# Kernel optimization log

Hardware: AMD Instinct MI355X
Metric: run time of the kernel (lower is better)

The kernel has to match this reference:

```python
import jax, jax.numpy as jnp
import numpy as np

B, H, T, D = 4, 16, 1024, 64
M = H * D  # model_dim = 1024
P = 2 * T - 1  # relative position length


def rel_shift(x):
    # x: (B, H, T, 2T-1) -> (B, H, T, T)
    b, h, t1, p = x.shape
    zero_pad = jnp.zeros((b, h, t1, 1), dtype=x.dtype)
    x_padded = jnp.concatenate([zero_pad, x], axis=-1)        # (B,H,T,2T)
    x_padded = x_padded.reshape(b, h, p + 1, t1)              # (B,H,2T,T)
    x = x_padded[:, :, 1:].reshape(b, h, t1, p)               # (B,H,T,2T-1)
    return x[:, :, :, : p // 2 + 1]                           # (B,H,T,T)


def setup_inputs() -> dict:
    key = jax.random.key(0)
    ks = jax.random.split(key, 7)
    q = jax.random.normal(ks[0], (B, H, T, D), dtype=jnp.float32)
    k = jax.random.normal(ks[1], (B, H, T, D), dtype=jnp.float32)
    v = jax.random.normal(ks[2], (B, H, T, D), dtype=jnp.float32)
    pos_emb = jax.random.normal(ks[3], (1, P, M), dtype=jnp.float32)
    attention_mask = jnp.ones((B, 1, 1, T), dtype=bool)
    # learned params
    W_pos = jax.random.normal(ks[4], (M, M), dtype=jnp.float32) * (M ** -0.5)
    pos_bias_u = jax.random.normal(ks[5], (H, D), dtype=jnp.float32) * 0.02
    pos_bias_v = jax.random.normal(ks[6], (H, D), dtype=jnp.float32) * 0.02
    return {"q": q, "k": k, "v": v, "pos_emb": pos_emb,
            "attention_mask": attention_mask, "W_pos": W_pos,
            "pos_bias_u": pos_bias_u, "pos_bias_v": pos_bias_v}


def reference(q, k, v, pos_emb, attention_mask, W_pos, pos_bias_u, pos_bias_v):
    # q, k, v: (B, H, T, D); pos_emb: (1, P, M)
    q_u = q + pos_bias_u[None, :, None, :]
    q_v = q + pos_bias_v[None, :, None, :]
    # linear_pos (no bias), split heads: (1, H, P, D)
    p = (pos_emb @ W_pos.T).reshape(pos_emb.shape[0], -1, H, D).transpose(0, 2, 1, 3)
    matrix_ac = jnp.einsum('bhqd,bhkd->bhqk', q_u, k)          # (B,H,T,T)
    matrix_bd = jnp.einsum('bhqd,hpd->bhqp', q_v, p[0])        # (B,H,T,P)
    matrix_bd = rel_shift(matrix_bd)                           # (B,H,T,T)
    scale = q.shape[-1] ** -0.5
    sim = (matrix_ac + matrix_bd) * scale
    sim = jnp.where(attention_mask, sim, jnp.finfo(sim.dtype).min)
    attn = jax.nn.softmax(sim, axis=-1)
    return jnp.einsum('bhqk,bhkd->bhqd', attn, v)
```

## Files before the change

kernel.cpp:

```cpp
#include <hip/hip_runtime.h>
#include <hip/hip_bf16.h>

#define BB 4
#define HH 16
#define TT 1024
#define DD 64
#define PP 2047
#define MM 1024

typedef __bf16 bf16;
typedef __bf16 bf16x8 __attribute__((ext_vector_type(8)));
typedef float  f32x4  __attribute__((ext_vector_type(4)));

__device__ inline bf16x8 pack8(float4 a, float4 b) {
    bf16x8 r;
    r[0]=(bf16)a.x; r[1]=(bf16)a.y; r[2]=(bf16)a.z; r[3]=(bf16)a.w;
    r[4]=(bf16)b.x; r[5]=(bf16)b.y; r[6]=(bf16)b.z; r[7]=(bf16)b.w;
    return r;
}

__device__ inline bf16x8 pack8_add_scale(float4 a, float4 b, float4 c, float4 d, float s) {
    bf16x8 r;
    r[0]=(bf16)((a.x+c.x)*s); r[1]=(bf16)((a.y+c.y)*s); r[2]=(bf16)((a.z+c.z)*s); r[3]=(bf16)((a.w+c.w)*s);
    r[4]=(bf16)((b.x+d.x)*s); r[5]=(bf16)((b.y+d.y)*s); r[6]=(bf16)((b.z+d.z)*s); r[7]=(bf16)((b.w+d.w)*s);
    return r;
}

__global__ __launch_bounds__(256) void cast_bf16_kernel(const float* __restrict__ src,
                                                        bf16* __restrict__ dst, int n8) {
    int i = blockIdx.x * 256 + threadIdx.x;
    if (i >= n8) return;
    const float4* s = (const float4*)src + (size_t)i * 2;
    ((bf16x8*)dst)[i] = pack8(s[0], s[1]);
}

__global__ __launch_bounds__(256) void transpose_v_kernel(const float* __restrict__ v,
                                                          bf16* __restrict__ vt) {
    __shared__ __attribute__((aligned(16))) bf16 Tld[64][72];
    const int t = threadIdx.x;
    const int bh = blockIdx.y;
    const int t0 = blockIdx.x * 64;
    {
        const int r = t >> 2, c0 = (t & 3) * 16;
        const float4* src = (const float4*)(v + ((size_t)bh * TT + t0 + r) * DD + c0);
        float4 a = src[0], b = src[1], c = src[2], d = src[3];
        *(bf16x8*)&Tld[r][c0]     = pack8(a, b);
        *(bf16x8*)&Tld[r][c0 + 8] = pack8(c, d);
    }
    __syncthreads();
    const int dd = t >> 2, j0l = (t & 3) * 16;
    bf16x8 o0, o1;
#pragma unroll
    for (int i = 0; i < 8; ++i) o0[i] = Tld[j0l + i][dd];
#pragma unroll
    for (int i = 0; i < 8; ++i) o1[i] = Tld[j0l + 8 + i][dd];
    bf16* dst = vt + ((size_t)bh * DD + dd) * TT + t0 + j0l;
    *(bf16x8*)dst = o0;
    *(bf16x8*)(dst + 8) = o1;
}

__global__ __launch_bounds__(256) void pos_gemm_kernel(const float* __restrict__ pos_emb,
                                                       const float* __restrict__ W_pos,
                                                       bf16* __restrict__ p_bf) {
    __shared__ __attribute__((aligned(16))) bf16 Abuf[64][72];
    __shared__ __attribute__((aligned(16))) bf16 Bbuf[128][72];
    const int t = threadIdx.x;
    const int w = t >> 6, lane = t & 63, quad = lane >> 4, col = lane & 15;
    const int wr = w >> 1, wc = w & 1;
    const int pp0 = blockIdx.x * 64;
    const int n0 = blockIdx.y * 128;

    f32x4 acc[2][4];
#pragma unroll
    for (int i = 0; i < 2; ++i)
#pragma unroll
        for (int j = 0; j < 4; ++j) acc[i][j] = (f32x4){0.f,0.f,0.f,0.f};

    for (int kt = 0; kt < 16; ++kt) {
        const int k0 = kt * 64;
        __syncthreads();
        {
            const int row = t >> 2, ch = (t & 3) * 16;
            const int pp = pp0 + row;
            if (pp < PP) {
                const float4* s = (const float4*)(pos_emb + (size_t)pp * MM + k0 + ch);
                float4 a = s[0], b = s[1], c = s[2], d = s[3];
                *(bf16x8*)&Abuf[row][ch]     = pack8(a, b);
                *(bf16x8*)&Abuf[row][ch + 8] = pack8(c, d);
            } else {
                float4 z = make_float4(0.f,0.f,0.f,0.f);
                *(bf16x8*)&Abuf[row][ch]     = pack8(z, z);
                *(bf16x8*)&Abuf[row][ch + 8] = pack8(z, z);
            }
        }
#pragma unroll
        for (int c = 0; c < 2; ++c) {
            const int idx = t * 2 + c;
            const int row = idx >> 2, ch = (idx & 3) * 16;
            const float4* s = (const float4*)(W_pos + (size_t)(n0 + row) * MM + k0 + ch);
            float4 a = s[0], b = s[1], cc = s[2], d = s[3];
            *(bf16x8*)&Bbuf[row][ch]     = pack8(a, b);
            *(bf16x8*)&Bbuf[row][ch + 8] = pack8(cc, d);
        }
        __syncthreads();
#pragma unroll
        for (int mt = 0; mt < 2; ++mt) {
            const int ar = wr * 32 + mt * 16 + col;
            const bf16x8 a0 = *(const bf16x8*)&Abuf[ar][quad * 8];
            const bf16x8 a1 = *(const bf16x8*)&Abuf[ar][32 + quad * 8];
#pragma unroll
            for (int nt = 0; nt < 4; ++nt) {
                const int br = wc * 64 + nt * 16 + col;
                const bf16x8 b0 = *(const bf16x8*)&Bbuf[br][quad * 8];
                const bf16x8 b1 = *(const bf16x8*)&Bbuf[br][32 + quad * 8];
                acc[mt][nt] = __builtin_amdgcn_mfma_f32_16x16x32_bf16(a0, b0, acc[mt][nt], 0, 0, 0);
                acc[mt][nt] = __builtin_amdgcn_mfma_f32_16x16x32_bf16(a1, b1, acc[mt][nt], 0, 0, 0);
            }
        }
    }
#pragma unroll
    for (int mt = 0; mt < 2; ++mt)
#pragma unroll
        for (int nt = 0; nt < 4; ++nt)
#pragma unroll
            for (int reg = 0; reg < 4; ++reg) {
                const int pp = pp0 + wr * 32 + mt * 16 + quad * 4 + reg;
                if (pp < PP) {
                    const int n = n0 + wc * 64 + nt * 16 + col;
                    p_bf[((size_t)(n >> 6) * PP + pp) * DD + (n & 63)] = (bf16)acc[mt][nt][reg];
                }
            }
}

__global__ __launch_bounds__(256, 4) void flash_kernel(const float* __restrict__ q,
                                                       const bf16* __restrict__ k_bf,
                                                       const bf16* __restrict__ vt_g,
                                                       const bf16* __restrict__ p_bf,
                                                       const float* __restrict__ bias_u,
                                                       const float* __restrict__ bias_v,
                                                       float* __restrict__ out) {
    __shared__ __attribute__((aligned(16))) bf16 Kld[64][72];
    __shared__ __attribute__((aligned(16))) bf16 Vt[64][72];
    __shared__ __attribute__((aligned(16))) bf16 Pwin[128][72];

    const int t = threadIdx.x;
    const int w = t >> 6, lane = t & 63, quad = lane >> 4, col = lane & 15;
    const int id = blockIdx.x;
    const int bh = ((id >> 7) << 3) | (id & 7);
    const int i0 = ((id >> 3) & 15) * 64;
    const int h = bh & 15;

    const float c1 = 0.18033688011112042f;

    bf16x8 quf[2], qvf[2];
    {
        const int rg = i0 + 16 * w + col;
        const float* qrow = q + ((size_t)bh * TT + rg) * DD;
        const float* urow = bias_u + h * DD;
        const float* vrow = bias_v + h * DD;
#pragma unroll
        for (int kk = 0; kk < 2; ++kk) {
            int off = kk * 32 + quad * 8;
            float4 f0 = *(const float4*)(qrow + off);
            float4 f1 = *(const float4*)(qrow + off + 4);
            float4 u0 = *(const float4*)(urow + off);
            float4 u1 = *(const float4*)(urow + off + 4);
            float4 v0 = *(const float4*)(vrow + off);
            float4 v1 = *(const float4*)(vrow + off + 4);
            quf[kk] = pack8_add_scale(f0, f1, u0, u1, c1);
            qvf[kk] = pack8_add_scale(f0, f1, v0, v1, c1);
        }
    }

    f32x4 acc[4] = {{0.f,0.f,0.f,0.f},{0.f,0.f,0.f,0.f},{0.f,0.f,0.f,0.f},{0.f,0.f,0.f,0.f}};
    float lpart[4] = {0.f, 0.f, 0.f, 0.f};

    const int sr = t >> 2, sc = (t & 3) * 16;

    for (int j0 = 0; j0 < TT; j0 += 64) {
        const int w0j = (TT - 64) + j0 - i0;
        __syncthreads();
        {
            const bf16x8* src = (const bf16x8*)(k_bf + ((size_t)bh * TT + j0 + sr) * DD + sc);
            *(bf16x8*)&Kld[sr][sc]     = src[0];
            *(bf16x8*)&Kld[sr][sc + 8] = src[1];
        }
#pragma unroll
        for (int c = 0; c < 2; ++c) {
            const int idx = t * 2 + c;
            const int dd = idx >> 3, ch = (idx & 7) * 8;
            *(bf16x8*)&Vt[dd][ch] =
                *(const bf16x8*)(vt_g + ((size_t)bh * DD + dd) * TT + j0 + ch);
        }
        if (j0 == 0) {
#pragma unroll
            for (int c = 0; c < 4; ++c) {
                const int idx = t * 4 + c;
                const int row = idx >> 3, ch = (idx & 7) * 8;
                const int pp = w0j + row;
                const int phys = pp & 127;
                if (pp < PP) {
                    *(bf16x8*)&Pwin[phys][ch] =
                        *(const bf16x8*)(p_bf + ((size_t)h * PP + pp) * DD + ch);
                } else {
                    float4 z = make_float4(0.f,0.f,0.f,0.f);
                    *(bf16x8*)&Pwin[phys][ch] = pack8(z, z);
                }
            }
        } else {
#pragma unroll
            for (int c = 0; c < 2; ++c) {
                const int idx = t * 2 + c;
                const int row = idx >> 3, ch = (idx & 7) * 8;
                const int pp = w0j + 64 + row;
                const int phys = pp & 127;
                if (pp < PP) {
                    *(bf16x8*)&Pwin[phys][ch] =
                        *(const bf16x8*)(p_bf + ((size_t)h * PP + pp) * DD + ch);
                } else {
                    float4 z = make_float4(0.f,0.f,0.f,0.f);
                    *(bf16x8*)&Pwin[phys][ch] = pack8(z, z);
                }
            }
        }
        __syncthreads();

        f32x4 s[4];
#pragma unroll
        for (int jt = 0; jt < 4; ++jt) {
            bf16x8 b0 = *(const bf16x8*)&Kld[jt * 16 + col][quad * 8];
            bf16x8 b1 = *(const bf16x8*)&Kld[jt * 16 + col][32 + quad * 8];
            f32x4 z = {0.f,0.f,0.f,0.f};
            z = __builtin_amdgcn_mfma_f32_16x16x32_bf16(quf[0], b0, z, 0, 0, 0);
            z = __builtin_amdgcn_mfma_f32_16x16x32_bf16(quf[1], b1, z, 0, 0, 0);
            s[jt] = z;
        }

        f32x4 zf[5];
#pragma unroll
        for (int f = 0; f < 5; ++f) {
            const int pp = w0j + (3 - w + f) * 16 + col;
            const int phys = pp & 127;
            bf16x8 b0 = *(const bf16x8*)&Pwin[phys][quad * 8];
            bf16x8 b1 = *(const bf16x8*)&Pwin[phys][32 + quad * 8];
            f32x4 z = {0.f,0.f,0.f,0.f};
            z = __builtin_amdgcn_mfma_f32_16x16x32_bf16(qvf[0], b0, z, 0, 0, 0);
            z = __builtin_amdgcn_mfma_f32_16x16x32_bf16(qvf[1], b1, z, 0, 0, 0);
            zf[f] = z;
        }

#pragma unroll
        for (int reg = 0; reg < 4; ++reg) {
            const int rl = quad * 4 + reg;
            const int srcc = (col + 15 - rl) & 15;
            const int idx = (((lane & 48) | srcc) << 2);
            float pm[5];
#pragma unroll
            for (int f = 0; f < 5; ++f)
                pm[f] = __int_as_float(__builtin_amdgcn_ds_bpermute(idx, __float_as_int(zf[f][reg])));
            const bool low = (col <= rl);
#pragma unroll
            for (int jt = 0; jt < 4; ++jt) {
                float x = s[jt][reg] + (low ? pm[jt] : pm[jt + 1]);
                float pv = exp2f(x);
                s[jt][reg] = pv;
                lpart[reg] += pv;
            }
        }
        __syncthreads();
#pragma unroll
        for (int reg = 0; reg < 4; ++reg) {
            const int rl = quad * 4 + reg;
#pragma unroll
            for (int jt = 0; jt < 4; ++jt)
                Kld[16 * w + rl][jt * 16 + col] = (bf16)s[jt][reg];
        }

#pragma unroll
        for (int kk = 0; kk < 2; ++kk) {
            bf16x8 af = *(const bf16x8*)&Kld[16 * w + col][kk * 32 + quad * 8];
#pragma unroll
            for (int jt = 0; jt < 4; ++jt) {
                bf16x8 bfv = *(const bf16x8*)&Vt[jt * 16 + col][kk * 32 + quad * 8];
                acc[jt] = __builtin_amdgcn_mfma_f32_16x16x32_bf16(af, bfv, acc[jt], 0, 0, 0);
            }
        }
    }

#pragma unroll
    for (int reg = 0; reg < 4; ++reg) {
        float lt = lpart[reg];
#pragma unroll
        for (int off = 1; off < 16; off <<= 1) lt += __shfl_xor(lt, off, 64);
        const float inv = 1.0f / lt;
        const int rg = i0 + 16 * w + quad * 4 + reg;
#pragma unroll
        for (int jt = 0; jt < 4; ++jt)
            out[((size_t)bh * TT + rg) * DD + jt * 16 + col] = acc[jt][reg] * inv;
    }
}

extern "C" void kernel_launch(void* const* d_in, const int* in_sizes, int n_in,
                              void* d_out, int out_size, void* d_ws, size_t ws_size,
                              hipStream_t stream) {
    const float* q       = (const float*)d_in[0];
    const float* k       = (const float*)d_in[1];
    const float* v       = (const float*)d_in[2];
    const float* pos_emb = (const float*)d_in[3];
    const float* W_pos   = (const float*)d_in[5];
    const float* bias_u  = (const float*)d_in[6];
    const float* bias_v  = (const float*)d_in[7];
    float* out = (float*)d_out;

    char* ws = (char*)d_ws;
    bf16* k_bf = (bf16*)(ws);
    bf16* vt_g = (bf16*)(ws + 8388608);
    bf16* p_bf = (bf16*)(ws + 16777216);

    const int n8 = (BB * HH * TT * DD) / 8;
    cast_bf16_kernel<<<n8 / 256, 256, 0, stream>>>(k, k_bf, n8);
    transpose_v_kernel<<<dim3(16, 64), 256, 0, stream>>>(v, vt_g);
    pos_gemm_kernel<<<dim3(32, 8), 256, 0, stream>>>(pos_emb, W_pos, p_bf);
    flash_kernel<<<1024, 256, 0, stream>>>(q, k_bf, vt_g, p_bf, bias_u, bias_v, out);
}
```

Baseline: 206.4 us.

## Give each wave 32 query rows and read K, V, P straight from global

Result: slower. 254.7 us (+23.4%).

```diff
diff --git a/kernel.cpp b/kernel.cpp
--- a/kernel.cpp
+++ b/kernel.cpp
@@ -132,29 +132,31 @@
             }
 }
 
-__global__ __launch_bounds__(256, 4) void flash_kernel(const float* __restrict__ q,
+__global__ __launch_bounds__(256, 3) void flash_kernel(const float* __restrict__ q,
                                                        const bf16* __restrict__ k_bf,
                                                        const bf16* __restrict__ vt_g,
                                                        const bf16* __restrict__ p_bf,
                                                        const float* __restrict__ bias_u,
                                                        const float* __restrict__ bias_v,
                                                        float* __restrict__ out) {
-    __shared__ __attribute__((aligned(16))) bf16 Kld[64][72];
-    __shared__ __attribute__((aligned(16))) bf16 Vt[64][72];
-    __shared__ __attribute__((aligned(16))) bf16 Pwin[128][72];
+    __shared__ __attribute__((aligned(16))) bf16 Sp[4][32][72];
 
     const int t = threadIdx.x;
     const int w = t >> 6, lane = t & 63, quad = lane >> 4, col = lane & 15;
     const int id = blockIdx.x;
-    const int bh = ((id >> 7) << 3) | (id & 7);
-    const int i0 = ((id >> 3) & 15) * 64;
+    const int bh = ((id >> 6) << 3) | (id & 7);
+    const int i0 = ((id >> 3) & 7) * 128;
     const int h = bh & 15;
 
     const float c1 = 0.18033688011112042f;
 
-    bf16x8 quf[2], qvf[2];
-    {
-        const int rg = i0 + 16 * w + col;
+    const int rs0 = i0 + 32 * w;
+    const int rs1 = rs0 + 16;
+
+    bf16x8 qu[2][2], qv[2][2];
+#pragma unroll
+    for (int s_ = 0; s_ < 2; ++s_) {
+        const int rg = rs0 + 16 * s_ + col;
         const float* qrow = q + ((size_t)bh * TT + rg) * DD;
         const float* urow = bias_u + h * DD;
         const float* vrow = bias_v + h * DD;
@@ -167,137 +169,111 @@
             float4 u1 = *(const float4*)(urow + off + 4);
             float4 v0 = *(const float4*)(vrow + off);
             float4 v1 = *(const float4*)(vrow + off + 4);
-            quf[kk] = pack8_add_scale(f0, f1, u0, u1, c1);
-            qvf[kk] = pack8_add_scale(f0, f1, v0, v1, c1);
+            qu[s_][kk] = pack8_add_scale(f0, f1, u0, u1, c1);
+            qv[s_][kk] = pack8_add_scale(f0, f1, v0, v1, c1);
         }
     }
 
-    f32x4 acc[4] = {{0.f,0.f,0.f,0.f},{0.f,0.f,0.f,0.f},{0.f,0.f,0.f,0.f},{0.f,0.f,0.f,0.f}};
-    float lpart[4] = {0.f, 0.f, 0.f, 0.f};
-
-    const int sr = t >> 2, sc = (t & 3) * 16;
+    f32x4 acc[2][4];
+#pragma unroll
+    for (int s_ = 0; s_ < 2; ++s_)
+#pragma unroll
+        for (int jt = 0; jt < 4; ++jt) acc[s_][jt] = (f32x4){0.f,0.f,0.f,0.f};
+    float lpart[2][4] = {{0.f,0.f,0.f,0.f},{0.f,0.f,0.f,0.f}};
+
+    const int srcc = (col + 15) & 15;
 
     for (int j0 = 0; j0 < TT; j0 += 64) {
-        const int w0j = (TT - 64) + j0 - i0;
-        __syncthreads();
-        {
-            const bf16x8* src = (const bf16x8*)(k_bf + ((size_t)bh * TT + j0 + sr) * DD + sc);
-            *(bf16x8*)&Kld[sr][sc]     = src[0];
-            *(bf16x8*)&Kld[sr][sc + 8] = src[1];
-        }
-#pragma unroll
-        for (int c = 0; c < 2; ++c) {
-            const int idx = t * 2 + c;
-            const int dd = idx >> 3, ch = (idx & 7) * 8;
-            *(bf16x8*)&Vt[dd][ch] =
-                *(const bf16x8*)(vt_g + ((size_t)bh * DD + dd) * TT + j0 + ch);
-        }
-        if (j0 == 0) {
-#pragma unroll
-            for (int c = 0; c < 4; ++c) {
-                const int idx = t * 4 + c;
-                const int row = idx >> 3, ch = (idx & 7) * 8;
-                const int pp = w0j + row;
-                const int phys = pp & 127;
-                if (pp < PP) {
-                    *(bf16x8*)&Pwin[phys][ch] =
-                        *(const bf16x8*)(p_bf + ((size_t)h * PP + pp) * DD + ch);
-                } else {
-                    float4 z = make_float4(0.f,0.f,0.f,0.f);
-                    *(bf16x8*)&Pwin[phys][ch] = pack8(z, z);
+        f32x4 s[2][4];
+#pragma unroll
+        for (int jt = 0; jt < 4; ++jt) {
+            const bf16* kr = k_bf + ((size_t)bh * TT + j0 + jt * 16 + col) * DD + quad * 8;
+            bf16x8 kb0 = *(const bf16x8*)kr;
+            bf16x8 kb1 = *(const bf16x8*)(kr + 32);
+            f32x4 z0 = {0.f,0.f,0.f,0.f};
+            z0 = __builtin_amdgcn_mfma_f32_16x16x32_bf16(qu[0][0], kb0, z0, 0, 0, 0);
+            z0 = __builtin_amdgcn_mfma_f32_16x16x32_bf16(qu[0][1], kb1, z0, 0, 0, 0);
+            s[0][jt] = z0;
+            f32x4 z1 = {0.f,0.f,0.f,0.f};
+            z1 = __builtin_amdgcn_mfma_f32_16x16x32_bf16(qu[1][0], kb0, z1, 0, 0, 0);
+            z1 = __builtin_amdgcn_mfma_f32_16x16x32_bf16(qu[1][1], kb1, z1, 0, 0, 0);
+            s[1][jt] = z1;
+        }
+
+        const int fb = (TT - 16) + j0 - rs1;
+        f32x4 zf1[5], zf0[5];
+#pragma unroll
+        for (int f = 0; f < 6; ++f) {
+            int pp = fb + 16 * f + col;
+            pp = min(max(pp, 0), PP - 1);
+            const bf16* pr = p_bf + ((size_t)h * PP + pp) * DD + quad * 8;
+            bf16x8 pb0 = *(const bf16x8*)pr;
+            bf16x8 pb1 = *(const bf16x8*)(pr + 32);
+            if (f < 5) {
+                f32x4 z = {0.f,0.f,0.f,0.f};
+                z = __builtin_amdgcn_mfma_f32_16x16x32_bf16(qv[1][0], pb0, z, 0, 0, 0);
+                z = __builtin_amdgcn_mfma_f32_16x16x32_bf16(qv[1][1], pb1, z, 0, 0, 0);
+                zf1[f] = z;
+            }
+            if (f >= 1) {
+                f32x4 z = {0.f,0.f,0.f,0.f};
+                z = __builtin_amdgcn_mfma_f32_16x16x32_bf16(qv[0][0], pb0, z, 0, 0, 0);
+                z = __builtin_amdgcn_mfma_f32_16x16x32_bf16(qv[0][1], pb1, z, 0, 0, 0);
+                zf0[f - 1] = z;
+            }
+        }
+
+#pragma unroll
+        for (int s_ = 0; s_ < 2; ++s_) {
+#pragma unroll
+            for (int reg = 0; reg < 4; ++reg) {
+                const int rl = quad * 4 + reg;
+                const int sc2 = (col + 15 - rl) & 15;
+                const int idx = (((lane & 48) | sc2) << 2);
+                float pm[5];
+#pragma unroll
+                for (int f = 0; f < 5; ++f) {
+                    const f32x4& zz = s_ ? zf1[f] : zf0[f];
+                    pm[f] = __int_as_float(__builtin_amdgcn_ds_bpermute(idx, __float_as_int(zz[reg])));
                 }
-            }
-        } else {
-#pragma unroll
-            for (int c = 0; c < 2; ++c) {
-                const int idx = t * 2 + c;
-                const int row = idx >> 3, ch = (idx & 7) * 8;
-                const int pp = w0j + 64 + row;
-                const int phys = pp & 127;
-                if (pp < PP) {
-                    *(bf16x8*)&Pwin[phys][ch] =
-                        *(const bf16x8*)(p_bf + ((size_t)h * PP + pp) * DD + ch);
-                } else {
-                    float4 z = make_float4(0.f,0.f,0.f,0.f);
-                    *(bf16x8*)&Pwin[phys][ch] = pack8(z, z);
+                const bool low = (col <= rl);
+#pragma unroll
+                for (int jt = 0; jt < 4; ++jt) {
+                    float x = s[s_][jt][reg] + (low ? pm[jt] : pm[jt + 1]);
+                    float pv = exp2f(x);
+                    lpart[s_][reg] += pv;
+                    Sp[w][16 * s_ + rl][jt * 16 + col] = (bf16)pv;
                 }
             }
         }
-        __syncthreads();
-
-        f32x4 s[4];
-#pragma unroll
-        for (int jt = 0; jt < 4; ++jt) {
-            bf16x8 b0 = *(const bf16x8*)&Kld[jt * 16 + col][quad * 8];
-            bf16x8 b1 = *(const bf16x8*)&Kld[jt * 16 + col][32 + quad * 8];
-            f32x4 z = {0.f,0.f,0.f,0.f};
-            z = __builtin_amdgcn_mfma_f32_16x16x32_bf16(quf[0], b0, z, 0, 0, 0);
-            z = __builtin_amdgcn_mfma_f32_16x16x32_bf16(quf[1], b1, z, 0, 0, 0);
-            s[jt] = z;
-        }
-
-        f32x4 zf[5];
-#pragma unroll
-        for (int f = 0; f < 5; ++f) {
-            const int pp = w0j + (3 - w + f) * 16 + col;
-            const int phys = pp & 127;
-            bf16x8 b0 = *(const bf16x8*)&Pwin[phys][quad * 8];
-            bf16x8 b1 = *(const bf16x8*)&Pwin[phys][32 + quad * 8];
-            f32x4 z = {0.f,0.f,0.f,0.f};
-            z = __builtin_amdgcn_mfma_f32_16x16x32_bf16(qvf[0], b0, z, 0, 0, 0);
-            z = __builtin_amdgcn_mfma_f32_16x16x32_bf16(qvf[1], b1, z, 0, 0, 0);
-            zf[f] = z;
-        }
-
+
+#pragma unroll
+        for (int kk = 0; kk < 2; ++kk) {
+            bf16x8 af0 = *(const bf16x8*)&Sp[w][col][kk * 32 + quad * 8];
+            bf16x8 af1 = *(const bf16x8*)&Sp[w][16 + col][kk * 32 + quad * 8];
+#pragma unroll
+            for (int jt = 0; jt < 4; ++jt) {
+                const bf16* vr = vt_g + ((size_t)bh * DD + jt * 16 + col) * TT + j0 + kk * 32 + quad * 8;
+                bf16x8 vb = *(const bf16x8*)vr;
+                acc[0][jt] = __builtin_amdgcn_mfma_f32_16x16x32_bf16(af0, vb, acc[0][jt], 0, 0, 0);
+                acc[1][jt] = __builtin_amdgcn_mfma_f32_16x16x32_bf16(af1, vb, acc[1][jt], 0, 0, 0);
+            }
+        }
+    }
+
+#pragma unroll
+    for (int s_ = 0; s_ < 2; ++s_)
 #pragma unroll
         for (int reg = 0; reg < 4; ++reg) {
-            const int rl = quad * 4 + reg;
-            const int srcc = (col + 15 - rl) & 15;
-            const int idx = (((lane & 48) | srcc) << 2);
-            float pm[5];
-#pragma unroll
-            for (int f = 0; f < 5; ++f)
-                pm[f] = __int_as_float(__builtin_amdgcn_ds_bpermute(idx, __float_as_int(zf[f][reg])));
-            const bool low = (col <= rl);
-#pragma unroll
-            for (int jt = 0; jt < 4; ++jt) {
-                float x = s[jt][reg] + (low ? pm[jt] : pm[jt + 1]);
-                float pv = exp2f(x);
-                s[jt][reg] = pv;
-                lpart[reg] += pv;
-            }
-        }
-        __syncthreads();
-#pragma unroll
-        for (int reg = 0; reg < 4; ++reg) {
-            const int rl = quad * 4 + reg;
+            float lt = lpart[s_][reg];
+#pragma unroll
+            for (int off = 1; off < 16; off <<= 1) lt += __shfl_xor(lt, off, 64);
+            const float inv = 1.0f / lt;
+            const int rg = rs0 + 16 * s_ + quad * 4 + reg;
 #pragma unroll
             for (int jt = 0; jt < 4; ++jt)
-                Kld[16 * w + rl][jt * 16 + col] = (bf16)s[jt][reg];
-        }
-
-#pragma unroll
-        for (int kk = 0; kk < 2; ++kk) {
-            bf16x8 af = *(const bf16x8*)&Kld[16 * w + col][kk * 32 + quad * 8];
-#pragma unroll
-            for (int jt = 0; jt < 4; ++jt) {
-                bf16x8 bfv = *(const bf16x8*)&Vt[jt * 16 + col][kk * 32 + quad * 8];
-                acc[jt] = __builtin_amdgcn_mfma_f32_16x16x32_bf16(af, bfv, acc[jt], 0, 0, 0);
-            }
-        }
-    }
-
-#pragma unroll
-    for (int reg = 0; reg < 4; ++reg) {
-        float lt = lpart[reg];
-#pragma unroll
-        for (int off = 1; off < 16; off <<= 1) lt += __shfl_xor(lt, off, 64);
-        const float inv = 1.0f / lt;
-        const int rg = i0 + 16 * w + quad * 4 + reg;
-#pragma unroll
-        for (int jt = 0; jt < 4; ++jt)
-            out[((size_t)bh * TT + rg) * DD + jt * 16 + col] = acc[jt][reg] * inv;
-    }
+                out[((size_t)bh * TT + rg) * DD + jt * 16 + col] = acc[s_][jt][reg] * inv;
+        }
 }
 
 extern "C" void kernel_launch(void* const* d_in, const int* in_sizes, int n_in,
@@ -321,5 +297,5 @@
     cast_bf16_kernel<<<n8 / 256, 256, 0, stream>>>(k, k_bf, n8);
     transpose_v_kernel<<<dim3(16, 64), 256, 0, stream>>>(v, vt_g);
     pos_gemm_kernel<<<dim3(32, 8), 256, 0, stream>>>(pos_emb, W_pos, p_bf);
-    flash_kernel<<<1024, 256, 0, stream>>>(q, k_bf, vt_g, p_bf, bias_u, bias_v, out);
-}
+    flash_kernel<<<512, 256, 0, stream>>>(q, k_bf, vt_g, p_bf, bias_u, bias_v, out);
+}
```
